# Optimization experiments

Measured on AMD Instinct MI355X. Metric: run time of the kernel, lower is better.

The kernel has to match this reference:

```python
import jax, jax.numpy as jnp
import numpy as np

M, D, NI, L, NPL, R, T = 2, 128, 131072, 4, 2048, 8, 32
N = NI + L * NPL  # total DAG nodes


def setup_inputs() -> dict:
    key = jax.random.key(0)
    ks = jax.random.split(key, 18)
    thax = jax.random.randint(ks[0], (NI,), 0, T)
    sine = jax.random.uniform(ks[1], (NI,), jnp.float32)
    # parents of layer-l deriv nodes index any node built earlier (topological)
    raw = jax.random.randint(ks[2], (L, NPL, 2), 0, 2**30)
    bounds = jnp.array([NI + l * NPL for l in range(L)])[:, None, None]
    par = raw % bounds
    ridx = jax.random.randint(ks[3], (L, NPL), 0, R)
    pos = jax.random.uniform(ks[4], (N,), jnp.float32) + 0.01
    neg = jax.random.uniform(ks[5], (N,), jnp.float32) + 0.01
    s = 0.05
    return {
        'thax': thax, 'sine': sine, 'par': par, 'ridx': ridx,
        'pos': pos, 'neg': neg,
        'init_table': jax.random.normal(ks[6], (M, T, D)) * s,
        's_vec': jax.random.normal(ks[7], (M, D)) * s,
        'W1': jax.random.normal(ks[8], (M, R, 2 * D, D)) * s,
        'b1': jax.random.normal(ks[9], (M, R, D)) * s,
        'W2': jax.random.normal(ks[10], (M, R, D, D)) * s,
        'b2': jax.random.normal(ks[11], (M, R, D)) * s,
        'tweaks': jax.random.normal(ks[12], (M, 1, 2)) * s,
        'We1': jax.random.normal(ks[13], (M, D, D)) * s,
        'be1': jax.random.normal(ks[14], (M, D)) * s,
        'we2': jax.random.normal(ks[15], (M, D)) * s,
        'be2': jax.random.normal(ks[16], (M,)) * s,
    }


def reference(thax, sine, par, ridx, pos, neg, init_table, s_vec,
              W1, b1, W2, b2, tweaks, We1, be1, we2, be2):
    # init nodes: thax embedding + sine embellishment (per model)
    emb0 = init_table[:, thax, :] + sine[None, :, None] * s_vec[:, None, :]  # [M,NI,D]
    store = jnp.zeros((M, N, D), emb0.dtype).at[:, :NI].set(emb0)
    # topological layers of deriv nodes: gather parents, rule-indexed 2-layer MLP
    for l in range(L):
        p, r = par[l], ridx[l]
        cat = store[:, p].reshape(M, NPL, 2 * D)               # gather parents
        h = jax.nn.relu(jnp.einsum('mnc,mncd->mnd', cat, W1[:, r]) + b1[:, r])
        out = (jnp.einsum('mnd,mnde->mne', h, W2[:, r]) + b2[:, r]
               + tweaks[:, 0, 1][:, None, None])
        store = store.at[:, NI + l * NPL: NI + (l + 1) * NPL].set(out)
    # eval_net: per-node scalar logit (+ per-problem tweak)
    he = jax.nn.relu(jnp.einsum('mnd,mde->mne', store, We1) + be1[:, None, :])
    logit = jnp.einsum('mnd,md->mn', he, we2) + be2[:, None] + tweaks[:, 0, 0][:, None]
    tot_pos, tot_neg = pos.sum(), neg.sum()
    pw = tot_neg / tot_pos  # POS_WEIGHT_EXTRA = 1.0
    gold = pos / (pos + neg)
    w = pos + neg
    # BCEWithLogitsLoss(pos_weight=pw) per node, weighted by (pos+neg)
    bce = -(pw * gold[None] * jax.nn.log_sigmoid(logit)
            + (1.0 - gold[None]) * jax.nn.log_sigmoid(-logit))
    loss = (w[None] * bce).sum(axis=1)                          # [M]
    posOK = jnp.where(logit >= 0, pos[None], 0.0).sum(axis=1)
    negOK = jnp.where(logit < 0, neg[None], 0.0).sum(axis=1)
    return (loss, posOK, negOK, tot_pos, tot_neg)
```

## Files before the change

### kernel.cpp

```cpp
#include <hip/hip_runtime.h>
#include <hip/hip_bf16.h>

#define M_ 2
#define D_ 128
#define NI_ 131072
#define L_ 4
#define NPL_ 2048
#define R_ 8
#define T_ 32
#define N_ (NI_ + L_ * NPL_)
#define ND_ (L_ * NPL_)
#define PART_ 640
#define FT_ 80

typedef __bf16 bf16x8 __attribute__((ext_vector_type(8)));
typedef float f32x4 __attribute__((ext_vector_type(4)));

#define OFF_W1T    0u
#define OFF_W2T    1048576u
#define OFF_WE1T   1572864u
#define OFF_TAB    1638400u
#define OFF_SVEC   1654784u
#define OFF_SORTED 1655296u
#define OFF_STARTS 1688064u
#define OFF_CNTF   1688192u
#define OFF_CNTA   1688320u
#define OFF_EA2    1688448u
#define OFF_EWB    1721216u
#define OFF_PA     1723264u
#define OFF_PB     1728384u
#define OFF_PPOK   1733504u
#define OFF_PNOK   1738624u
#define OFF_PTP    1743744u
#define OFF_PTN    1746304u
#define OFF_G      1748864u
#define OFF_STORE  2289536u
#define OFF_FSG    6483840u
#define OFF_CFG    6483872u
#define OFF_FLIST  6483904u

__device__ __forceinline__ unsigned short f2bu(float f) {
  unsigned int u = __float_as_uint(f);
  u += 0x7fffu + ((u >> 16) & 1u);
  return (unsigned short)(u >> 16);
}
__device__ __forceinline__ bf16x8 ldb8(const unsigned short* p) {
  return *reinterpret_cast<const bf16x8*>(p);
}

__device__ __forceinline__ bf16x8 node_chunk(int m, int row, int d0,
    const unsigned short* tab, const unsigned short* svec,
    const unsigned short* sd, const int* thax, const float* sine) {
  if (row < NI_) {
    bf16x8 tv = ldb8(&tab[(m * T_ + thax[row]) * D_ + d0]);
    bf16x8 sv = ldb8(&svec[m * D_ + d0]);
    float sn = sine[row];
    bf16x8 r;
#pragma unroll
    for (int j = 0; j < 8; ++j)
      r[j] = (__bf16)((float)tv[j] + sn * (float)sv[j]);
    return r;
  }
  return ldb8(&sd[(size_t)(m * ND_ + (row - NI_)) * D_ + d0]);
}

__global__ __launch_bounds__(256) void megaprep_kernel(
    const float* W1, const float* W2, const float* We1,
    const float* init_table, const float* s_vec,
    const float* b1, const float* be1, const float* we2,
    const int* ridx, const int* par,
    unsigned short* W1T, unsigned short* W2T, unsigned short* We1T,
    unsigned short* tab, unsigned short* svec,
    float* G, float* EA2, float* EWB,
    int* sorted, int* starts, int* cntF, int* cntA,
    int* fsg, int* cfg, int* fastlist) {
  __shared__ float smem[1056];
  __shared__ int icnt[16], ioff[16];
  int job = blockIdx.x;
  int tid = threadIdx.x;

  if (job < 800) {
    int z, rblk, cblk;
    if (job < 512)      { z = job >> 5;            rblk = (job & 31) >> 2; cblk = job & 3; }
    else if (job < 768) { int q = job - 512; z = 16 + (q >> 4); rblk = (q & 15) >> 2; cblk = q & 3; }
    else                { int q = job - 768; z = 32 + (q >> 4); rblk = (q & 15) >> 2; cblk = q & 3; }
    const float* src; unsigned short* dst; int R;
    if (z < 16)      { src = W1  + (size_t)z * 32768;        dst = W1T  + (size_t)z * 32768;        R = 256; }
    else if (z < 32) { src = W2  + (size_t)(z - 16) * 16384; dst = W2T  + (size_t)(z - 16) * 16384; R = 128; }
    else             { src = We1 + (size_t)(z - 32) * 16384; dst = We1T + (size_t)(z - 32) * 16384; R = 128; }
    int r0 = rblk * 32, c0 = cblk * 32;
    float (*tile)[33] = (float(*)[33])smem;
    int tx = tid & 31, ty = tid >> 5;
#pragma unroll
    for (int k = 0; k < 4; ++k)
      tile[ty + 8 * k][tx] = src[(size_t)(r0 + ty + 8 * k) * D_ + c0 + tx];
    __syncthreads();
#pragma unroll
    for (int k = 0; k < 4; ++k)
      dst[(size_t)(c0 + ty + 8 * k) * R + r0 + tx] = f2bu(tile[tx][ty + 8 * k]);
  } else if (job == 800) {
    for (int i = tid; i < 8448; i += 256) {
      if (i < 8192) tab[i] = f2bu(init_table[i]);
      else svec[i - 8192] = f2bu(s_vec[i - 8192]);
    }
  } else if (job < 1329) {
    int q = job - 801;
    int t = q / 16, mr = q & 15;
    int m = mr >> 3;
    int slot = tid >> 7, e = tid & 127;
    const float* vec = (t < 32) ? &init_table[(size_t)(m * T_ + t) * D_]
                                : &s_vec[(size_t)m * D_];
    if (tid < 128) smem[tid] = vec[tid];
    __syncthreads();
    const float* w = &W1[((size_t)mr * 256 + slot * 128) * D_];
    float acc = 0.f;
#pragma unroll 8
    for (int c = 0; c < 128; ++c) acc = fmaf(smem[c], w[c * D_ + e], acc);
    if (slot == 0 && t < 32) acc += b1[mr * D_ + e];
    G[((size_t)(mr * 2 + slot) * 33 + t) * D_ + e] = acc;
  } else if (job < 1363) {
    int q = job - 1329;
    int m = q / 17, t = (q % 17) * 2 + (tid >> 7);
    int e = tid & 127;
    if (t <= 32) {
      const float* vec = (t < 32) ? &init_table[(size_t)(m * T_ + t) * D_]
                                  : &s_vec[(size_t)m * D_];
      const float* w = &We1[(size_t)m * D_ * D_];
      float acc = 0.f;
#pragma unroll 8
      for (int d = 0; d < 128; ++d) acc = fmaf(vec[d], w[d * D_ + e], acc);
      if (t < 32) {
        EA2[m * 4096 + ((e >> 1) * 32 + t) * 2 + (e & 1)] = acc + be1[m * D_ + e];
      } else {
        EWB[(m * D_ + e) * 2 + 0] = acc;
        EWB[(m * D_ + e) * 2 + 1] = we2[m * D_ + e];
      }
    }
  } else if (job < 1367) {
    int l = job - 1363;
    if (tid < 16) icnt[tid] = 0;
    __syncthreads();
    for (int n = tid; n < NPL_; n += 256) {
      int r = ridx[l * NPL_ + n];
      int p0 = par[(l * NPL_ + n) * 2 + 0], p1 = par[(l * NPL_ + n) * 2 + 1];
      int slow = (p0 >= NI_ || p1 >= NI_) ? 1 : 0;
      atomicAdd(&icnt[r * 2 + slow], 1);
    }
    __syncthreads();
    if (tid == 0) {
      int run = 0;
      for (int b = 0; b < 16; ++b) { ioff[b] = run; run += icnt[b]; }
      for (int r = 0; r < R_; ++r) {
        starts[l * R_ + r] = ioff[2 * r];
        cntF[l * R_ + r] = icnt[2 * r];
        cntA[l * R_ + r] = icnt[2 * r] + icnt[2 * r + 1];
      }
    }
    __syncthreads();
    for (int n = tid; n < NPL_; n += 256) {
      int r = ridx[l * NPL_ + n];
      int p0 = par[(l * NPL_ + n) * 2 + 0], p1 = par[(l * NPL_ + n) * 2 + 1];
      int slow = (p0 >= NI_ || p1 >= NI_) ? 1 : 0;
      int p = atomicAdd(&ioff[r * 2 + slow], 1);
      sorted[l * NPL_ + p] = n;
    }
  } else {
    if (tid < 8) icnt[tid] = 0;
    __syncthreads();
    for (int g = tid; g < ND_; g += 256) {
      int p0 = par[2 * g], p1 = par[2 * g + 1];
      if (p0 < NI_ && p1 < NI_) atomicAdd(&icnt[ridx[g]], 1);
    }
    __syncthreads();
    if (tid == 0) {
      int run = 0;
      for (int r = 0; r < R_; ++r) {
        ioff[r] = run; fsg[r] = run; cfg[r] = icnt[r]; run += icnt[r];
      }
    }
    __syncthreads();
    for (int g = tid; g < ND_; g += 256) {
      int p0 = par[2 * g], p1 = par[2 * g + 1];
      if (p0 < NI_ && p1 < NI_) {
        int p = atomicAdd(&ioff[ridx[g]], 1);
        fastlist[p] = g;
      }
    }
  }
}

__global__ __launch_bounds__(256) void main_kernel(
    const int* thax, const float* sine, const int* par,
    const float* pos, const float* neg,
    const float* b2, const float* tweaks,
    const float* G, const unsigned short* W2T,
    const float* EA2, const float* EWB, const float* be2,
    const int* fsg, const int* cfg, const int* fastlist,
    unsigned short* sd,
    float* pA, float* pB, float* pPok, float* pNok, float* pTp, float* pTn) {
  __shared__ float sbuf[4448];
  int bid = blockIdx.x;
  int tid = threadIdx.x;
  int w = tid >> 6, lane = tid & 63;

  if (bid < 1280) {
    int m = bid / 640, q = bid % 640;
    int r = q / 80, tile = q % 80;
    int cnt = cfg[r];
    int base = tile * 16;
    if (base >= cnt) return;
    unsigned short* h_lds = (unsigned short*)sbuf;
    int*   t0a  = (int*)(sbuf + 1024);
    int*   t1a  = t0a + 16;
    float* s0a  = (float*)(t1a + 16);
    float* s1a  = s0a + 16;
    int*   gida = (int*)(s1a + 16);
    if (tid < 16) {
      int loc = base + tid; if (loc >= cnt) loc = cnt - 1;
      int gid = fastlist[fsg[r] + loc];
      int p0 = par[2 * gid], p1 = par[2 * gid + 1];
      t0a[tid] = thax[p0]; s0a[tid] = sine[p0];
      t1a[tid] = thax[p1]; s1a[tid] = sine[p1];
      gida[tid] = gid;
    }
    __syncthreads();
    const float* Gm = &G[(size_t)(m * R_ + r) * 8448];
    {
      int row = tid >> 4, seg = tid & 15, d0 = seg * 8;
      int t0 = t0a[row], t1 = t1a[row];
      float s0 = s0a[row], s1 = s1a[row];
      const float* pa = &Gm[t0 * 128 + d0];
      const float* pb = &Gm[(33 + t1) * 128 + d0];
      const float* pu = &Gm[4096 + d0];
      const float* pv = &Gm[8320 + d0];
      bf16x8 hv;
#pragma unroll
      for (int half = 0; half < 2; ++half) {
        float4 a = *(const float4*)(pa + half * 4);
        float4 b = *(const float4*)(pb + half * 4);
        float4 u = *(const float4*)(pu + half * 4);
        float4 v = *(const float4*)(pv + half * 4);
        hv[half * 4 + 0] = (__bf16)fmaxf(a.x + b.x + s0 * u.x + s1 * v.x, 0.f);
        hv[half * 4 + 1] = (__bf16)fmaxf(a.y + b.y + s0 * u.y + s1 * v.y, 0.f);
        hv[half * 4 + 2] = (__bf16)fmaxf(a.z + b.z + s0 * u.z + s1 * v.z, 0.f);
        hv[half * 4 + 3] = (__bf16)fmaxf(a.w + b.w + s0 * u.w + s1 * v.w, 0.f);
      }
      *(bf16x8*)&h_lds[row * 128 + (d0 ^ ((row & 7) << 3))] = hv;
    }
    __syncthreads();
    int l15 = lane & 15, l4 = lane >> 4;
    const unsigned short* w2b = &W2T[(size_t)(m * R_ + r) * D_ * D_];
    f32x4 acc[2];
    acc[0] = (f32x4){0.f, 0.f, 0.f, 0.f};
    acc[1] = (f32x4){0.f, 0.f, 0.f, 0.f};
#pragma unroll
    for (int kc = 0; kc < 4; ++kc) {
      int d0 = kc * 32 + l4 * 8;
      bf16x8 a2 = ldb8(&h_lds[l15 * 128 + (d0 ^ ((l15 & 7) << 3))]);
#pragma unroll
      for (int f = 0; f < 2; ++f) {
        int fg = w * 2 + f;
        bf16x8 b = ldb8(&w2b[(fg * 16 + l15) * D_ + d0]);
        acc[f] = __builtin_amdgcn_mfma_f32_16x16x32_bf16(a2, b, acc[f], 0, 0, 0);
      }
    }
    float tw1 = tweaks[m * 2 + 1];
    const float* b2v = &b2[(m * R_ + r) * D_];
#pragma unroll
    for (int i = 0; i < 4; ++i) {
      int g = base + l4 * 4 + i;
      if (g < cnt) {
        int gid = gida[l4 * 4 + i];
        unsigned short* dst = &sd[(size_t)(m * ND_ + gid) * D_];
#pragma unroll
        for (int f = 0; f < 2; ++f) {
          int e = (w * 2 + f) * 16 + l15;
          dst[e] = f2bu(acc[f][i] + b2v[e] + tw1);
        }
      }
    }
  } else {
    int q = bid - 1280;
    int m = q >> 9, xb = q & 511;
    float* lea = sbuf;
    float* lwb = sbuf + 4096;
    float* red = sbuf + 4352;
    for (int i = tid; i < 4096; i += 256) lea[i] = EA2[m * 4096 + i];
    if (tid < 256) lwb[tid] = EWB[m * 256 + tid];
    __syncthreads();
    int row = xb * 256 + tid;
    int t = thax[row];
    float s = sine[row];
    float acc = 0.f;
#pragma unroll 8
    for (int p = 0; p < 64; ++p) {
      float2 ea = *(const float2*)&lea[(p * 32 + t) * 2];
      float4 wb = *(const float4*)&lwb[p * 4];
      float x0 = fmaf(s, wb.x, ea.x); x0 = fmaxf(x0, 0.f);
      acc = fmaf(x0, wb.y, acc);
      float x1 = fmaf(s, wb.z, ea.y); x1 = fmaxf(x1, 0.f);
      acc = fmaf(x1, wb.w, acc);
    }
    float logit = acc + be2[m] + tweaks[m * 2 + 0];
    float p_ = pos[row], n_ = neg[row];
    float lse = log1pf(__expf(-fabsf(logit)));
    float v[6];
    v[0] = p_ * (fmaxf(-logit, 0.f) + lse);
    v[1] = n_ * (fmaxf(logit, 0.f) + lse);
    v[2] = logit >= 0.f ? p_ : 0.f;
    v[3] = logit < 0.f ? n_ : 0.f;
    v[4] = p_; v[5] = n_;
#pragma unroll
    for (int mask = 1; mask < 64; mask <<= 1) {
#pragma unroll
      for (int k = 0; k < 6; ++k) v[k] += __shfl_xor(v[k], mask, 64);
    }
    if (lane == 0) {
#pragma unroll
      for (int k = 0; k < 6; ++k) red[k * 16 + w] = v[k];
    }
    __syncthreads();
    if (tid == 0) {
      float t6[6];
#pragma unroll
      for (int k = 0; k < 6; ++k)
        t6[k] = red[k * 16 + 0] + red[k * 16 + 1] + red[k * 16 + 2] + red[k * 16 + 3];
      pA[m * PART_ + xb] = t6[0];
      pB[m * PART_ + xb] = t6[1];
      pPok[m * PART_ + xb] = t6[2];
      pNok[m * PART_ + xb] = t6[3];
      if (m == 0) { pTp[xb] = t6[4]; pTn[xb] = t6[5]; }
    }
  }
}

__global__ __launch_bounds__(128) void slow_kernel(int l,
    const int* thax, const float* sine, const int* par,
    const float* b1, const float* b2, const float* tweaks,
    const unsigned short* tab, const unsigned short* svec,
    const unsigned short* W1T, const unsigned short* W2T,
    const int* sorted, const int* starts, const int* cntF, const int* cntA,
    unsigned short* sd) {
  int tile = blockIdx.x, r = blockIdx.y, m = blockIdx.z;
  int cF = cntF[l * R_ + r];
  int cS = cntA[l * R_ + r] - cF;
  int base = tile * 16;
  if (base >= cS) return;
  int start = starts[l * R_ + r] + cF;
  int tid = threadIdx.x;
  int w = tid >> 6, lane = tid & 63;
  int l15 = lane & 15, l4 = lane >> 4;
  __shared__ unsigned short h_lds[16 * 128];

  int loc = base + l15; if (loc >= cS) loc = cS - 1;
  int node = sorted[l * NPL_ + start + loc];
  int p0 = par[(l * NPL_ + node) * 2 + 0];
  int p1 = par[(l * NPL_ + node) * 2 + 1];
  const unsigned short* w1b = &W1T[(size_t)(m * R_ + r) * D_ * 256];
  const unsigned short* w2b = &W2T[(size_t)(m * R_ + r) * D_ * D_];

  bf16x8 av[8];
#pragma unroll
  for (int kc = 0; kc < 8; ++kc) {
    int k = kc * 32 + l4 * 8;
    int p = (k < 128) ? p0 : p1;
    av[kc] = node_chunk(m, p, k & 127, tab, svec, sd, thax, sine);
  }
  f32x4 acch[4];
#pragma unroll
  for (int f = 0; f < 4; ++f) acch[f] = (f32x4){0.f, 0.f, 0.f, 0.f};
#pragma unroll
  for (int kc = 0; kc < 8; ++kc) {
    int k = kc * 32 + l4 * 8;
#pragma unroll
    for (int f = 0; f < 4; ++f) {
      int fg = w * 4 + f;
      bf16x8 b = ldb8(&w1b[(fg * 16 + l15) * 256 + k]);
      acch[f] = __builtin_amdgcn_mfma_f32_16x16x32_bf16(av[kc], b, acch[f], 0, 0, 0);
    }
  }
  const float* b1v = &b1[(m * R_ + r) * D_];
#pragma unroll
  for (int f = 0; f < 4; ++f) {
    int d = (w * 4 + f) * 16 + l15;
    float bb = b1v[d];
#pragma unroll
    for (int i = 0; i < 4; ++i) {
      int row = l4 * 4 + i;
      float h = acch[f][i] + bb;
      h = h > 0.f ? h : 0.f;
      h_lds[row * 128 + (d ^ ((row & 7) << 3))] = f2bu(h);
    }
  }
  __syncthreads();
  f32x4 acco[4];
#pragma unroll
  for (int f = 0; f < 4; ++f) acco[f] = (f32x4){0.f, 0.f, 0.f, 0.f};
#pragma unroll
  for (int kc = 0; kc < 4; ++kc) {
    int d0 = kc * 32 + l4 * 8;
    bf16x8 a2 = ldb8(&h_lds[l15 * 128 + (d0 ^ ((l15 & 7) << 3))]);
#pragma unroll
    for (int f = 0; f < 4; ++f) {
      int fg = w * 4 + f;
      bf16x8 b = ldb8(&w2b[(fg * 16 + l15) * D_ + d0]);
      acco[f] = __builtin_amdgcn_mfma_f32_16x16x32_bf16(a2, b, acco[f], 0, 0, 0);
    }
  }
  float tw1 = tweaks[m * 2 + 1];
  const float* b2v = &b2[(m * R_ + r) * D_];
#pragma unroll
  for (int i = 0; i < 4; ++i) {
    int g = base + l4 * 4 + i;
    if (g < cS) {
      int nd = sorted[l * NPL_ + start + g];
      unsigned short* dst = &sd[(size_t)(m * ND_ + l * NPL_ + nd) * D_];
#pragma unroll
      for (int f = 0; f < 4; ++f) {
        int e = (w * 4 + f) * 16 + l15;
        dst[e] = f2bu(acco[f][i] + b2v[e] + tw1);
      }
    }
  }
}

__global__ __launch_bounds__(256) void evald_kernel(
    const float* pos, const float* neg,
    const float* be1, const float* we2, const float* be2, const float* tweaks,
    const unsigned short* We1T, const unsigned short* sd,
    float* pA, float* pB, float* pPok, float* pNok, float* pTp, float* pTn) {
  int tile = blockIdx.x, m = blockIdx.y;
  int tid = threadIdx.x;
  int w = tid >> 6, lane = tid & 63;
  int l15 = lane & 15, l4 = lane >> 4;
  int rbase = tile * 64 + w * 16;
  int arow = rbase + l15;
  __shared__ float red[6][16];

  bf16x8 a[4];
#pragma unroll
  for (int kc = 0; kc < 4; ++kc)
    a[kc] = ldb8(&sd[((size_t)m * ND_ + arow) * D_ + kc * 32 + l4 * 8]);
  f32x4 acc[8];
#pragma unroll
  for (int f = 0; f < 8; ++f) acc[f] = (f32x4){0.f, 0.f, 0.f, 0.f};
#pragma unroll
  for (int kc = 0; kc < 4; ++kc) {
#pragma unroll
    for (int f = 0; f < 8; ++f) {
      bf16x8 b = ldb8(&We1T[(m * D_ + f * 16 + l15) * D_ + kc * 32 + l4 * 8]);
      acc[f] = __builtin_amdgcn_mfma_f32_16x16x32_bf16(a[kc], b, acc[f], 0, 0, 0);
    }
  }
  float part[4] = {0.f, 0.f, 0.f, 0.f};
#pragma unroll
  for (int f = 0; f < 8; ++f) {
    int e = f * 16 + l15;
    float bb = be1[m * D_ + e];
    float wv = we2[m * D_ + e];
#pragma unroll
    for (int i = 0; i < 4; ++i) {
      float he = acc[f][i] + bb;
      he = he > 0.f ? he : 0.f;
      part[i] += he * wv;
    }
  }
#pragma unroll
  for (int mask = 1; mask < 16; mask <<= 1) {
#pragma unroll
    for (int i = 0; i < 4; ++i) part[i] += __shfl_xor(part[i], mask, 64);
  }
  if (l15 == 0) {
    float tw0 = tweaks[m * 2 + 0];
    float bev = be2[m];
    float sa = 0.f, sb = 0.f, spok = 0.f, snok = 0.f, stp = 0.f, stn = 0.f;
#pragma unroll
    for (int i = 0; i < 4; ++i) {
      int row = NI_ + rbase + l4 * 4 + i;
      float logit = part[i] + bev + tw0;
      float p = pos[row], ng = neg[row];
      float lse = log1pf(__expf(-fabsf(logit)));
      sa += p * (fmaxf(-logit, 0.f) + lse);
      sb += ng * (fmaxf(logit, 0.f) + lse);
      if (logit >= 0.f) spok += p; else snok += ng;
      stp += p; stn += ng;
    }
    int slot = w * 4 + l4;
    red[0][slot] = sa;   red[1][slot] = sb;
    red[2][slot] = spok; red[3][slot] = snok;
    red[4][slot] = stp;  red[5][slot] = stn;
  }
  __syncthreads();
  if (tid == 0) {
    float t6[6];
#pragma unroll
    for (int q = 0; q < 6; ++q) {
      float s = 0.f;
      for (int k = 0; k < 16; ++k) s += red[q][k];
      t6[q] = s;
    }
    int slot = 512 + tile;
    pA[m * PART_ + slot] = t6[0];
    pB[m * PART_ + slot] = t6[1];
    pPok[m * PART_ + slot] = t6[2];
    pNok[m * PART_ + slot] = t6[3];
    if (m == 0) { pTp[slot] = t6[4]; pTn[slot] = t6[5]; }
  }
}

__global__ __launch_bounds__(256) void finalize_kernel(
    const float* pA, const float* pB, const float* pPok, const float* pNok,
    const float* pTp, const float* pTn, float* out) {
  __shared__ float lred[10][4];
  const float* srcs[10] = {pA, pA + PART_, pB, pB + PART_,
                           pPok, pPok + PART_, pNok, pNok + PART_,
                           pTp, pTn};
  int tid = threadIdx.x;
  int w = tid >> 6, lane = tid & 63;
#pragma unroll
  for (int q = 0; q < 10; ++q) {
    float s = 0.f;
    for (int i = tid; i < PART_; i += 256) s += srcs[q][i];
#pragma unroll
    for (int mask = 1; mask < 64; mask <<= 1) s += __shfl_xor(s, mask, 64);
    if (lane == 0) lred[q][w] = s;
  }
  __syncthreads();
  if (tid == 0) {
    float totals[10];
#pragma unroll
    for (int q = 0; q < 10; ++q)
      totals[q] = lred[q][0] + lred[q][1] + lred[q][2] + lred[q][3];
    float tp = totals[8], tn = totals[9];
    float pw = tn / tp;
    out[0] = pw * totals[0] + totals[2];
    out[1] = pw * totals[1] + totals[3];
    out[2] = totals[4]; out[3] = totals[5];
    out[4] = totals[6]; out[5] = totals[7];
    out[6] = tp; out[7] = tn;
  }
}

extern "C" void kernel_launch(void* const* d_in, const int* in_sizes, int n_in,
                              void* d_out, int out_size, void* d_ws, size_t ws_size,
                              hipStream_t stream) {
  const int*   thax = (const int*)d_in[0];
  const float* sine = (const float*)d_in[1];
  const int*   par  = (const int*)d_in[2];
  const int*   ridx = (const int*)d_in[3];
  const float* pos  = (const float*)d_in[4];
  const float* neg  = (const float*)d_in[5];
  const float* init_table = (const float*)d_in[6];
  const float* s_vec = (const float*)d_in[7];
  const float* W1 = (const float*)d_in[8];
  const float* b1 = (const float*)d_in[9];
  const float* W2 = (const float*)d_in[10];
  const float* b2 = (const float*)d_in[11];
  const float* tweaks = (const float*)d_in[12];
  const float* We1 = (const float*)d_in[13];
  const float* be1 = (const float*)d_in[14];
  const float* we2 = (const float*)d_in[15];
  const float* be2 = (const float*)d_in[16];

  char* ws = (char*)d_ws;
  unsigned short* W1T  = (unsigned short*)(ws + OFF_W1T);
  unsigned short* W2T  = (unsigned short*)(ws + OFF_W2T);
  unsigned short* We1T = (unsigned short*)(ws + OFF_WE1T);
  unsigned short* tab  = (unsigned short*)(ws + OFF_TAB);
  unsigned short* svec = (unsigned short*)(ws + OFF_SVEC);
  int* sorted = (int*)(ws + OFF_SORTED);
  int* starts = (int*)(ws + OFF_STARTS);
  int* cntF   = (int*)(ws + OFF_CNTF);
  int* cntA   = (int*)(ws + OFF_CNTA);
  float* EA2  = (float*)(ws + OFF_EA2);
  float* EWB  = (float*)(ws + OFF_EWB);
  float* pA   = (float*)(ws + OFF_PA);
  float* pB   = (float*)(ws + OFF_PB);
  float* pPok = (float*)(ws + OFF_PPOK);
  float* pNok = (float*)(ws + OFF_PNOK);
  float* pTp  = (float*)(ws + OFF_PTP);
  float* pTn  = (float*)(ws + OFF_PTN);
  float* G    = (float*)(ws + OFF_G);
  unsigned short* sd = (unsigned short*)(ws + OFF_STORE);
  int* fsg      = (int*)(ws + OFF_FSG);
  int* cfg      = (int*)(ws + OFF_CFG);
  int* fastlist = (int*)(ws + OFF_FLIST);

  megaprep_kernel<<<1368, 256, 0, stream>>>(
      W1, W2, We1, init_table, s_vec, b1, be1, we2, ridx, par,
      W1T, W2T, We1T, tab, svec, G, EA2, EWB, sorted, starts, cntF, cntA,
      fsg, cfg, fastlist);
  main_kernel<<<2304, 256, 0, stream>>>(
      thax, sine, par, pos, neg, b2, tweaks, G, W2T, EA2, EWB, be2,
      fsg, cfg, fastlist, sd, pA, pB, pPok, pNok, pTp, pTn);
  for (int l = 1; l < L_; ++l) {
    slow_kernel<<<dim3(8, R_, M_), 128, 0, stream>>>(
        l, thax, sine, par, b1, b2, tweaks, tab, svec, W1T, W2T,
        sorted, starts, cntF, cntA, sd);
  }
  evald_kernel<<<dim3(128, M_), 256, 0, stream>>>(
      pos, neg, be1, we2, be2, tweaks, We1T, sd,
      pA, pB, pPok, pNok, pTp, pTn);
  finalize_kernel<<<1, 256, 0, stream>>>(pA, pB, pPok, pNok, pTp, pTn,
                                         (float*)d_out);
}
```

Measured before the change: 99.26 us.

## Fuse slow layers, eval and finalize into one persistent kernel with grid barriers

Replaces the three per-layer slow_kernel launches plus the evald and finalize launches with a single 256-block persistent tail_kernel. Dependencies between layers and stages are enforced by atomic-counter grid barriers, whose counters are reset in megaprep. The slow-layer work now uses 256-thread blocks, each computing 2 output fragments per wave instead of 4. This removes four kernel launch gaps at the cost of spin-wait barriers. The barriers rely on all 256 blocks being co-resident and have a spin cap that could silently break ordering.

```diff
diff --git a/kernel.cpp b/kernel.cpp
--- a/kernel.cpp
+++ b/kernel.cpp
@@ -11,7 +11,6 @@
 #define N_ (NI_ + L_ * NPL_)
 #define ND_ (L_ * NPL_)
 #define PART_ 640
-#define FT_ 80
 
 typedef __bf16 bf16x8 __attribute__((ext_vector_type(8)));
 typedef float f32x4 __attribute__((ext_vector_type(4)));
@@ -38,6 +37,7 @@
 #define OFF_FSG    6483840u
 #define OFF_CFG    6483872u
 #define OFF_FLIST  6483904u
+#define OFF_BAR    6516672u
 
 __device__ __forceinline__ unsigned short f2bu(float f) {
   unsigned int u = __float_as_uint(f);
@@ -46,6 +46,22 @@
 }
 __device__ __forceinline__ bf16x8 ldb8(const unsigned short* p) {
   return *reinterpret_cast<const bf16x8*>(p);
+}
+
+__device__ __forceinline__ void gbar(int* slot, int nb) {
+  __syncthreads();
+  if (threadIdx.x == 0) {
+    __threadfence();
+    __hip_atomic_fetch_add(slot, 1, __ATOMIC_ACQ_REL, __HIP_MEMORY_SCOPE_AGENT);
+    int spins = 0;
+    while (__hip_atomic_load(slot, __ATOMIC_ACQUIRE, __HIP_MEMORY_SCOPE_AGENT) < nb
+           && spins < (1 << 20)) {
+      __builtin_amdgcn_s_sleep(1);
+      ++spins;
+    }
+    __threadfence();
+  }
+  __syncthreads();
 }
 
 __device__ __forceinline__ bf16x8 node_chunk(int m, int row, int d0,
@@ -73,7 +89,7 @@
     unsigned short* tab, unsigned short* svec,
     float* G, float* EA2, float* EWB,
     int* sorted, int* starts, int* cntF, int* cntA,
-    int* fsg, int* cfg, int* fastlist) {
+    int* fsg, int* cfg, int* fastlist, int* bar) {
   __shared__ float smem[1056];
   __shared__ int icnt[16], ioff[16];
   int job = blockIdx.x;
@@ -99,6 +115,7 @@
     for (int k = 0; k < 4; ++k)
       dst[(size_t)(c0 + ty + 8 * k) * R + r0 + tx] = f2bu(tile[tx][ty + 8 * k]);
   } else if (job == 800) {
+    if (tid < 8) bar[tid] = 0;
     for (int i = tid; i < 8448; i += 256) {
       if (i < 8192) tab[i] = f2bu(init_table[i]);
       else svec[i - 8192] = f2bu(s_vec[i - 8192]);
@@ -334,210 +351,211 @@
   }
 }
 
-__global__ __launch_bounds__(128) void slow_kernel(int l,
+__global__ __launch_bounds__(256) void tail_kernel(
     const int* thax, const float* sine, const int* par,
     const float* b1, const float* b2, const float* tweaks,
+    const float* pos, const float* neg,
+    const float* be1, const float* we2, const float* be2,
     const unsigned short* tab, const unsigned short* svec,
     const unsigned short* W1T, const unsigned short* W2T,
+    const unsigned short* We1T,
     const int* sorted, const int* starts, const int* cntF, const int* cntA,
-    unsigned short* sd) {
-  int tile = blockIdx.x, r = blockIdx.y, m = blockIdx.z;
-  int cF = cntF[l * R_ + r];
-  int cS = cntA[l * R_ + r] - cF;
-  int base = tile * 16;
-  if (base >= cS) return;
-  int start = starts[l * R_ + r] + cF;
+    unsigned short* sd, int* bar,
+    float* pA, float* pB, float* pPok, float* pNok, float* pTp, float* pTn,
+    float* out) {
+  __shared__ unsigned short h_lds[16 * 128];
+  __shared__ float red[6][16];
+  __shared__ float lred[10][4];
+  int bid = blockIdx.x;
   int tid = threadIdx.x;
+  int nb = gridDim.x;
   int w = tid >> 6, lane = tid & 63;
   int l15 = lane & 15, l4 = lane >> 4;
-  __shared__ unsigned short h_lds[16 * 128];
-
-  int loc = base + l15; if (loc >= cS) loc = cS - 1;
-  int node = sorted[l * NPL_ + start + loc];
-  int p0 = par[(l * NPL_ + node) * 2 + 0];
-  int p1 = par[(l * NPL_ + node) * 2 + 1];
-  const unsigned short* w1b = &W1T[(size_t)(m * R_ + r) * D_ * 256];
-  const unsigned short* w2b = &W2T[(size_t)(m * R_ + r) * D_ * D_];
-
-  bf16x8 av[8];
-#pragma unroll
-  for (int kc = 0; kc < 8; ++kc) {
-    int k = kc * 32 + l4 * 8;
-    int p = (k < 128) ? p0 : p1;
-    av[kc] = node_chunk(m, p, k & 127, tab, svec, sd, thax, sine);
+
+  for (int l = 1; l < L_; ++l) {
+    if (bid < 128) {
+      int tile = bid & 7, r = (bid >> 3) & 7, m = bid >> 6;
+      int cF = cntF[l * R_ + r];
+      int cS = cntA[l * R_ + r] - cF;
+      int base = tile * 16;
+      if (base < cS) {
+        int start = starts[l * R_ + r] + cF;
+        int loc = base + l15; if (loc >= cS) loc = cS - 1;
+        int node = sorted[l * NPL_ + start + loc];
+        int p0 = par[(l * NPL_ + node) * 2 + 0];
+        int p1 = par[(l * NPL_ + node) * 2 + 1];
+        const unsigned short* w1b = &W1T[(size_t)(m * R_ + r) * D_ * 256];
+        const unsigned short* w2b = &W2T[(size_t)(m * R_ + r) * D_ * D_];
+        bf16x8 av[8];
+#pragma unroll
+        for (int kc = 0; kc < 8; ++kc) {
+          int k = kc * 32 + l4 * 8;
+          int p = (k < 128) ? p0 : p1;
+          av[kc] = node_chunk(m, p, k & 127, tab, svec, sd, thax, sine);
+        }
+        f32x4 acch[2];
+        acch[0] = (f32x4){0.f, 0.f, 0.f, 0.f};
+        acch[1] = (f32x4){0.f, 0.f, 0.f, 0.f};
+#pragma unroll
+        for (int kc = 0; kc < 8; ++kc) {
+          int k = kc * 32 + l4 * 8;
+#pragma unroll
+          for (int f = 0; f < 2; ++f) {
+            int fg = w * 2 + f;
+            bf16x8 b = ldb8(&w1b[(fg * 16 + l15) * 256 + k]);
+            acch[f] = __builtin_amdgcn_mfma_f32_16x16x32_bf16(av[kc], b, acch[f], 0, 0, 0);
+          }
+        }
+        const float* b1v = &b1[(m * R_ + r) * D_];
+#pragma unroll
+        for (int f = 0; f < 2; ++f) {
+          int d = (w * 2 + f) * 16 + l15;
+          float bb = b1v[d];
+#pragma unroll
+          for (int i = 0; i < 4; ++i) {
+            int row = l4 * 4 + i;
+            float h = acch[f][i] + bb;
+            h = h > 0.f ? h : 0.f;
+            h_lds[row * 128 + (d ^ ((row & 7) << 3))] = f2bu(h);
+          }
+        }
+        __syncthreads();
+        f32x4 acco[2];
+        acco[0] = (f32x4){0.f, 0.f, 0.f, 0.f};
+        acco[1] = (f32x4){0.f, 0.f, 0.f, 0.f};
+#pragma unroll
+        for (int kc = 0; kc < 4; ++kc) {
+          int d0 = kc * 32 + l4 * 8;
+          bf16x8 a2 = ldb8(&h_lds[l15 * 128 + (d0 ^ ((l15 & 7) << 3))]);
+#pragma unroll
+          for (int f = 0; f < 2; ++f) {
+            int fg = w * 2 + f;
+            bf16x8 b = ldb8(&w2b[(fg * 16 + l15) * D_ + d0]);
+            acco[f] = __builtin_amdgcn_mfma_f32_16x16x32_bf16(a2, b, acco[f], 0, 0, 0);
+          }
+        }
+        float tw1 = tweaks[m * 2 + 1];
+        const float* b2v = &b2[(m * R_ + r) * D_];
+#pragma unroll
+        for (int i = 0; i < 4; ++i) {
+          int g = base + l4 * 4 + i;
+          if (g < cS) {
+            int nd = sorted[l * NPL_ + start + g];
+            unsigned short* dst = &sd[(size_t)(m * ND_ + l * NPL_ + nd) * D_];
+#pragma unroll
+            for (int f = 0; f < 2; ++f) {
+              int e = (w * 2 + f) * 16 + l15;
+              dst[e] = f2bu(acco[f][i] + b2v[e] + tw1);
+            }
+          }
+        }
+      }
+    }
+    gbar(&bar[l - 1], nb);
   }
-  f32x4 acch[4];
-#pragma unroll
-  for (int f = 0; f < 4; ++f) acch[f] = (f32x4){0.f, 0.f, 0.f, 0.f};
-#pragma unroll
-  for (int kc = 0; kc < 8; ++kc) {
-    int k = kc * 32 + l4 * 8;
-#pragma unroll
-    for (int f = 0; f < 4; ++f) {
-      int fg = w * 4 + f;
-      bf16x8 b = ldb8(&w1b[(fg * 16 + l15) * 256 + k]);
-      acch[f] = __builtin_amdgcn_mfma_f32_16x16x32_bf16(av[kc], b, acch[f], 0, 0, 0);
+
+  {
+    int m = bid >> 7, tile = bid & 127;
+    int rbase = tile * 64 + w * 16;
+    int arow = rbase + l15;
+    bf16x8 a[4];
+#pragma unroll
+    for (int kc = 0; kc < 4; ++kc)
+      a[kc] = ldb8(&sd[((size_t)m * ND_ + arow) * D_ + kc * 32 + l4 * 8]);
+    f32x4 acc[8];
+#pragma unroll
+    for (int f = 0; f < 8; ++f) acc[f] = (f32x4){0.f, 0.f, 0.f, 0.f};
+#pragma unroll
+    for (int kc = 0; kc < 4; ++kc) {
+#pragma unroll
+      for (int f = 0; f < 8; ++f) {
+        bf16x8 b = ldb8(&We1T[(m * D_ + f * 16 + l15) * D_ + kc * 32 + l4 * 8]);
+        acc[f] = __builtin_amdgcn_mfma_f32_16x16x32_bf16(a[kc], b, acc[f], 0, 0, 0);
+      }
+    }
+    float part[4] = {0.f, 0.f, 0.f, 0.f};
+#pragma unroll
+    for (int f = 0; f < 8; ++f) {
+      int e = f * 16 + l15;
+      float bb = be1[m * D_ + e];
+      float wv = we2[m * D_ + e];
+#pragma unroll
+      for (int i = 0; i < 4; ++i) {
+        float he = acc[f][i] + bb;
+        he = he > 0.f ? he : 0.f;
+        part[i] += he * wv;
+      }
+    }
+#pragma unroll
+    for (int mask = 1; mask < 16; mask <<= 1) {
+#pragma unroll
+      for (int i = 0; i < 4; ++i) part[i] += __shfl_xor(part[i], mask, 64);
+    }
+    if (l15 == 0) {
+      float tw0 = tweaks[m * 2 + 0];
+      float bev = be2[m];
+      float sa = 0.f, sb = 0.f, spok = 0.f, snok = 0.f, stp = 0.f, stn = 0.f;
+#pragma unroll
+      for (int i = 0; i < 4; ++i) {
+        int row = NI_ + rbase + l4 * 4 + i;
+        float logit = part[i] + bev + tw0;
+        float p = pos[row], ng = neg[row];
+        float lse = log1pf(__expf(-fabsf(logit)));
+        sa += p * (fmaxf(-logit, 0.f) + lse);
+        sb += ng * (fmaxf(logit, 0.f) + lse);
+        if (logit >= 0.f) spok += p; else snok += ng;
+        stp += p; stn += ng;
+      }
+      int slot = w * 4 + l4;
+      red[0][slot] = sa;   red[1][slot] = sb;
+      red[2][slot] = spok; red[3][slot] = snok;
+      red[4][slot] = stp;  red[5][slot] = stn;
+    }
+    __syncthreads();
+    if (tid == 0) {
+      float t6[6];
+#pragma unroll
+      for (int q = 0; q < 6; ++q) {
+        float s = 0.f;
+        for (int k = 0; k < 16; ++k) s += red[q][k];
+        t6[q] = s;
+      }
+      int slot = 512 + tile;
+      pA[m * PART_ + slot] = t6[0];
+      pB[m * PART_ + slot] = t6[1];
+      pPok[m * PART_ + slot] = t6[2];
+      pNok[m * PART_ + slot] = t6[3];
+      if (m == 0) { pTp[slot] = t6[4]; pTn[slot] = t6[5]; }
     }
   }
-  const float* b1v = &b1[(m * R_ + r) * D_];
-#pragma unroll
-  for (int f = 0; f < 4; ++f) {
-    int d = (w * 4 + f) * 16 + l15;
-    float bb = b1v[d];
-#pragma unroll
-    for (int i = 0; i < 4; ++i) {
-      int row = l4 * 4 + i;
-      float h = acch[f][i] + bb;
-      h = h > 0.f ? h : 0.f;
-      h_lds[row * 128 + (d ^ ((row & 7) << 3))] = f2bu(h);
-    }
-  }
-  __syncthreads();
-  f32x4 acco[4];
-#pragma unroll
-  for (int f = 0; f < 4; ++f) acco[f] = (f32x4){0.f, 0.f, 0.f, 0.f};
-#pragma unroll
-  for (int kc = 0; kc < 4; ++kc) {
-    int d0 = kc * 32 + l4 * 8;
-    bf16x8 a2 = ldb8(&h_lds[l15 * 128 + (d0 ^ ((l15 & 7) << 3))]);
-#pragma unroll
-    for (int f = 0; f < 4; ++f) {
-      int fg = w * 4 + f;
-      bf16x8 b = ldb8(&w2b[(fg * 16 + l15) * D_ + d0]);
-      acco[f] = __builtin_amdgcn_mfma_f32_16x16x32_bf16(a2, b, acco[f], 0, 0, 0);
-    }
-  }
-  float tw1 = tweaks[m * 2 + 1];
-  const float* b2v = &b2[(m * R_ + r) * D_];
-#pragma unroll
-  for (int i = 0; i < 4; ++i) {
-    int g = base + l4 * 4 + i;
-    if (g < cS) {
-      int nd = sorted[l * NPL_ + start + g];
-      unsigned short* dst = &sd[(size_t)(m * ND_ + l * NPL_ + nd) * D_];
-#pragma unroll
-      for (int f = 0; f < 4; ++f) {
-        int e = (w * 4 + f) * 16 + l15;
-        dst[e] = f2bu(acco[f][i] + b2v[e] + tw1);
-      }
-    }
-  }
-}
-
-__global__ __launch_bounds__(256) void evald_kernel(
-    const float* pos, const float* neg,
-    const float* be1, const float* we2, const float* be2, const float* tweaks,
-    const unsigned short* We1T, const unsigned short* sd,
-    float* pA, float* pB, float* pPok, float* pNok, float* pTp, float* pTn) {
-  int tile = blockIdx.x, m = blockIdx.y;
-  int tid = threadIdx.x;
-  int w = tid >> 6, lane = tid & 63;
-  int l15 = lane & 15, l4 = lane >> 4;
-  int rbase = tile * 64 + w * 16;
-  int arow = rbase + l15;
-  __shared__ float red[6][16];
-
-  bf16x8 a[4];
-#pragma unroll
-  for (int kc = 0; kc < 4; ++kc)
-    a[kc] = ldb8(&sd[((size_t)m * ND_ + arow) * D_ + kc * 32 + l4 * 8]);
-  f32x4 acc[8];
-#pragma unroll
-  for (int f = 0; f < 8; ++f) acc[f] = (f32x4){0.f, 0.f, 0.f, 0.f};
-#pragma unroll
-  for (int kc = 0; kc < 4; ++kc) {
-#pragma unroll
-    for (int f = 0; f < 8; ++f) {
-      bf16x8 b = ldb8(&We1T[(m * D_ + f * 16 + l15) * D_ + kc * 32 + l4 * 8]);
-      acc[f] = __builtin_amdgcn_mfma_f32_16x16x32_bf16(a[kc], b, acc[f], 0, 0, 0);
-    }
-  }
-  float part[4] = {0.f, 0.f, 0.f, 0.f};
-#pragma unroll
-  for (int f = 0; f < 8; ++f) {
-    int e = f * 16 + l15;
-    float bb = be1[m * D_ + e];
-    float wv = we2[m * D_ + e];
-#pragma unroll
-    for (int i = 0; i < 4; ++i) {
-      float he = acc[f][i] + bb;
-      he = he > 0.f ? he : 0.f;
-      part[i] += he * wv;
-    }
-  }
-#pragma unroll
-  for (int mask = 1; mask < 16; mask <<= 1) {
-#pragma unroll
-    for (int i = 0; i < 4; ++i) part[i] += __shfl_xor(part[i], mask, 64);
-  }
-  if (l15 == 0) {
-    float tw0 = tweaks[m * 2 + 0];
-    float bev = be2[m];
-    float sa = 0.f, sb = 0.f, spok = 0.f, snok = 0.f, stp = 0.f, stn = 0.f;
-#pragma unroll
-    for (int i = 0; i < 4; ++i) {
-      int row = NI_ + rbase + l4 * 4 + i;
-      float logit = part[i] + bev + tw0;
-      float p = pos[row], ng = neg[row];
-      float lse = log1pf(__expf(-fabsf(logit)));
-      sa += p * (fmaxf(-logit, 0.f) + lse);
-      sb += ng * (fmaxf(logit, 0.f) + lse);
-      if (logit >= 0.f) spok += p; else snok += ng;
-      stp += p; stn += ng;
-    }
-    int slot = w * 4 + l4;
-    red[0][slot] = sa;   red[1][slot] = sb;
-    red[2][slot] = spok; red[3][slot] = snok;
-    red[4][slot] = stp;  red[5][slot] = stn;
-  }
-  __syncthreads();
-  if (tid == 0) {
-    float t6[6];
-#pragma unroll
-    for (int q = 0; q < 6; ++q) {
+  gbar(&bar[3], nb);
+
+  if (bid == 0) {
+    const float* srcs[10] = {pA, pA + PART_, pB, pB + PART_,
+                             pPok, pPok + PART_, pNok, pNok + PART_,
+                             pTp, pTn};
+#pragma unroll
+    for (int q = 0; q < 10; ++q) {
       float s = 0.f;
-      for (int k = 0; k < 16; ++k) s += red[q][k];
-      t6[q] = s;
-    }
-    int slot = 512 + tile;
-    pA[m * PART_ + slot] = t6[0];
-    pB[m * PART_ + slot] = t6[1];
-    pPok[m * PART_ + slot] = t6[2];
-    pNok[m * PART_ + slot] = t6[3];
-    if (m == 0) { pTp[slot] = t6[4]; pTn[slot] = t6[5]; }
-  }
-}
-
-__global__ __launch_bounds__(256) void finalize_kernel(
-    const float* pA, const float* pB, const float* pPok, const float* pNok,
-    const float* pTp, const float* pTn, float* out) {
-  __shared__ float lred[10][4];
-  const float* srcs[10] = {pA, pA + PART_, pB, pB + PART_,
-                           pPok, pPok + PART_, pNok, pNok + PART_,
-                           pTp, pTn};
-  int tid = threadIdx.x;
-  int w = tid >> 6, lane = tid & 63;
-#pragma unroll
-  for (int q = 0; q < 10; ++q) {
-    float s = 0.f;
-    for (int i = tid; i < PART_; i += 256) s += srcs[q][i];
-#pragma unroll
-    for (int mask = 1; mask < 64; mask <<= 1) s += __shfl_xor(s, mask, 64);
-    if (lane == 0) lred[q][w] = s;
-  }
-  __syncthreads();
-  if (tid == 0) {
-    float totals[10];
-#pragma unroll
-    for (int q = 0; q < 10; ++q)
-      totals[q] = lred[q][0] + lred[q][1] + lred[q][2] + lred[q][3];
-    float tp = totals[8], tn = totals[9];
-    float pw = tn / tp;
-    out[0] = pw * totals[0] + totals[2];
-    out[1] = pw * totals[1] + totals[3];
-    out[2] = totals[4]; out[3] = totals[5];
-    out[4] = totals[6]; out[5] = totals[7];
-    out[6] = tp; out[7] = tn;
+      for (int i = tid; i < PART_; i += 256) s += srcs[q][i];
+#pragma unroll
+      for (int mask = 1; mask < 64; mask <<= 1) s += __shfl_xor(s, mask, 64);
+      if (lane == 0) lred[q][w] = s;
+    }
+    __syncthreads();
+    if (tid == 0) {
+      float totals[10];
+#pragma unroll
+      for (int q = 0; q < 10; ++q)
+        totals[q] = lred[q][0] + lred[q][1] + lred[q][2] + lred[q][3];
+      float tp = totals[8], tn = totals[9];
+      float pw = tn / tp;
+      out[0] = pw * totals[0] + totals[2];
+      out[1] = pw * totals[1] + totals[3];
+      out[2] = totals[4]; out[3] = totals[5];
+      out[4] = totals[6]; out[5] = totals[7];
+      out[6] = tp; out[7] = tn;
+    }
   }
 }
 
@@ -585,22 +603,17 @@
   int* fsg      = (int*)(ws + OFF_FSG);
   int* cfg      = (int*)(ws + OFF_CFG);
   int* fastlist = (int*)(ws + OFF_FLIST);
+  int* bar      = (int*)(ws + OFF_BAR);
 
   megaprep_kernel<<<1368, 256, 0, stream>>>(
       W1, W2, We1, init_table, s_vec, b1, be1, we2, ridx, par,
       W1T, W2T, We1T, tab, svec, G, EA2, EWB, sorted, starts, cntF, cntA,
-      fsg, cfg, fastlist);
+      fsg, cfg, fastlist, bar);
   main_kernel<<<2304, 256, 0, stream>>>(
       thax, sine, par, pos, neg, b2, tweaks, G, W2T, EA2, EWB, be2,
       fsg, cfg, fastlist, sd, pA, pB, pPok, pNok, pTp, pTn);
-  for (int l = 1; l < L_; ++l) {
-    slow_kernel<<<dim3(8, R_, M_), 128, 0, stream>>>(
-        l, thax, sine, par, b1, b2, tweaks, tab, svec, W1T, W2T,
-        sorted, starts, cntF, cntA, sd);
-  }
-  evald_kernel<<<dim3(128, M_), 256, 0, stream>>>(
-      pos, neg, be1, we2, be2, tweaks, We1T, sd,
-      pA, pB, pPok, pNok, pTp, pTn);
-  finalize_kernel<<<1, 256, 0, stream>>>(pA, pB, pPok, pNok, pTp, pTn,
-                                         (float*)d_out);
-}
+  tail_kernel<<<256, 256, 0, stream>>>(
+      thax, sine, par, b1, b2, tweaks, pos, neg, be1, we2, be2,
+      tab, svec, W1T, W2T, We1T, sorted, starts, cntF, cntA,
+      sd, bar, pA, pB, pPok, pNok, pTp, pTn, (float*)d_out);
+}
```

Result: slower. 208.6 us (+110.2%).
